# Kernel optimization log

Measured on AMD Instinct MI355X. Metric: run time of the kernel, lower is better.

The kernel has to match this reference:

```python
import jax, jax.numpy as jnp
import numpy as np

N_NODES = 100000


def _gcn_norm(edges, n_nodes):
    # PyG GCNConv: add self-loops, symmetric normalization D^{-1/2}(A+I)D^{-1/2}
    loop = jnp.arange(n_nodes, dtype=edges.dtype)
    src = jnp.concatenate([edges[0], loop])
    dst = jnp.concatenate([edges[1], loop])
    ones = jnp.ones(src.shape[0], dtype=jnp.float32)
    deg = jax.ops.segment_sum(ones, dst, num_segments=n_nodes)  # >=1 thanks to self-loops
    dinv = jax.lax.rsqrt(deg)
    norm = dinv[src] * dinv[dst]  # [E + N]
    return src, dst, norm


def _gcn_conv(x, W, b, src, dst, norm, n_nodes):
    # lin -> gather -> scale -> scatter-add -> +bias (PyG GCNConv order)
    h = x @ W                                   # [N, D_out]
    msg = h[src] * norm[:, None]                # [E+N, D_out]
    agg = jax.ops.segment_sum(msg, dst, num_segments=n_nodes)
    return agg + b


def setup_inputs() -> dict:
    key = jax.random.key(0)
    k_x, k_e, k_w1, k_w2 = jax.random.split(key, 4)
    F_in, D_hid, n_labels, n_edges = 128, 128, 32, 625000
    features = jax.random.normal(k_x, (N_NODES, F_in), dtype=jnp.float32)
    edges = jax.random.randint(k_e, (2, n_edges), 0, N_NODES, dtype=jnp.int64)
    W1 = jax.random.normal(k_w1, (F_in, D_hid), dtype=jnp.float32) / np.sqrt(F_in)
    b1 = jnp.zeros((D_hid,), dtype=jnp.float32)
    W2 = jax.random.normal(k_w2, (D_hid, n_labels), dtype=jnp.float32) / np.sqrt(D_hid)
    b2 = jnp.zeros((n_labels,), dtype=jnp.float32)
    return {"features": features, "edges": edges, "W1": W1, "b1": b1, "W2": W2, "b2": b2}


def reference(features, edges, W1, b1, W2, b2):
    n_nodes = features.shape[0]
    src, dst, norm = _gcn_norm(edges, n_nodes)
    h1 = jax.nn.relu(_gcn_conv(features, W1, b1, src, dst, norm, n_nodes))
    h2 = _gcn_conv(h1, W2, b2, src, dst, norm, n_nodes)
    return jax.nn.log_softmax(h2, axis=1)
```

## Files before the change

### kernel.cpp

```cpp
#include <hip/hip_runtime.h>

#define NN 100000
#define MAXDEG 64

typedef _Float16 f16;
typedef f16 f16x2 __attribute__((ext_vector_type(2)));
typedef f16 f16x8 __attribute__((ext_vector_type(8)));
typedef float f32x4 __attribute__((ext_vector_type(4)));

__device__ __forceinline__ int detect_is64(const void* edges, int E) {
    const long long* p = (const long long*)edges;
    int m = E < 1024 ? E : 1024;
    int bad = 0;
    for (int i = (threadIdx.x & 63); i < m; i += 64) {
        if ((unsigned long long)p[i] >= (unsigned long long)NN) bad = 1;
    }
    return !__any(bad);
}

__device__ __forceinline__ int edge_at(const void* e, long i, int is64) {
    return is64 ? (int)((const long long*)e)[i] : ((const int*)e)[i];
}

__global__ __launch_bounds__(256) void k_prep(const float* __restrict__ W1,
                                              const float* __restrict__ W2,
                                              f16* __restrict__ BT1,
                                              f16* __restrict__ BT2,
                                              int* __restrict__ deg, int n) {
    int t = blockIdx.x * blockDim.x + threadIdx.x;
    int stride = gridDim.x * blockDim.x;
    for (int i = t; i < n; i += stride) deg[i] = 0;
    for (int i = t; i < 128 * 128; i += stride) {
        int nn = i >> 7, kk = i & 127;
        BT1[i] = (f16)W1[kk * 128 + nn];
    }
    for (int i = t; i < 32 * 128; i += stride) {
        int nn = i >> 7, kk = i & 127;
        BT2[i] = (f16)W2[kk * 32 + nn];
    }
}

__global__ __launch_bounds__(256) void k_geb(const float* __restrict__ X,
                                             const f16* __restrict__ BT,
                                             f16* __restrict__ H, int n,
                                             const void* edges, int E,
                                             int* __restrict__ deg,
                                             int* __restrict__ csr,
                                             int nG, int nF) {
    __shared__ __align__(16) unsigned char Bs[16384];
    const int bid = blockIdx.x;
    const int lo = nG < nF ? nG : nF;
    int gid = -1, fid = -1;
    if (bid < 2 * lo) {
        if ((bid & 1) == 0) gid = bid >> 1; else fid = bid >> 1;
    } else if (nG > nF) {
        gid = bid - lo;
    } else {
        fid = bid - lo;
    }

    if (fid >= 0) {
        int is64 = detect_is64(edges, E);
        long stride = (long)nF * 256;
        for (long e = (long)fid * 256 + threadIdx.x; e < E; e += stride) {
            int s = edge_at(edges, e, is64);
            int d = edge_at(edges, (long)E + e, is64);
            int t = atomicAdd(&deg[d], 1);
            if (t < MAXDEG) csr[(long)d * MAXDEG + t] = s;
        }
        return;
    }

    const int tid = threadIdx.x;
    const int wave = tid >> 6;
    const int lane = tid & 63;
    const int lrow = lane & 15;
    const int kgrp = lane >> 4;
    const int row0 = gid * 64 + wave * 16;
    int arow = row0 + lrow;
    if (arow >= n) arow = n - 1;

    f16x8 a[4];
#pragma unroll
    for (int ks = 0; ks < 4; ks++) {
        const float* ap = &X[(long)arow * 128 + ks * 32 + kgrp * 8];
        float4 v0 = *(const float4*)ap;
        float4 v1 = *(const float4*)(ap + 4);
        f16x8 tv;
        tv[0] = (f16)v0.x; tv[1] = (f16)v0.y; tv[2] = (f16)v0.z; tv[3] = (f16)v0.w;
        tv[4] = (f16)v1.x; tv[5] = (f16)v1.y; tv[6] = (f16)v1.z; tv[7] = (f16)v1.w;
        a[ks] = tv;
    }

    const int sw = (lrow & 7) << 4;
#pragma unroll
    for (int half = 0; half < 2; half++) {
#pragma unroll
        for (int s = 0; s < 4; s++) {
            int L = (tid + s * 256) * 16;
            int row = L >> 8;
            f16x8 v = *(const f16x8*)((const unsigned char*)BT + half * 16384 + L);
            *(f16x8*)(Bs + (L ^ ((row & 7) << 4))) = v;
        }
        __syncthreads();
#pragma unroll
        for (int ntl = 0; ntl < 4; ntl++) {
            f32x4 acc = {0.f, 0.f, 0.f, 0.f};
            const int bbase = (ntl * 16 + lrow) * 256 + kgrp * 16;
#pragma unroll
            for (int ks = 0; ks < 4; ks++) {
                f16x8 b = *(const f16x8*)(Bs + ((bbase + ks * 64) ^ sw));
                acc = __builtin_amdgcn_mfma_f32_16x16x32_f16(a[ks], b, acc, 0, 0, 0);
            }
            const int col = (half * 4 + ntl) * 16 + lrow;
#pragma unroll
            for (int r = 0; r < 4; r++) {
                int grow = row0 + kgrp * 4 + r;
                if (grow < n) H[(long)grow * 128 + col] = (f16)acc[r];
            }
        }
        __syncthreads();
    }
}

__global__ __launch_bounds__(256) void k_gemm2(const f16* __restrict__ A,
                                               const f16* __restrict__ BT,
                                               f16* __restrict__ H, int n) {
    __shared__ __align__(16) unsigned char Bs[8192];
    const int tid = threadIdx.x;
    {
        int L = tid * 16;
        int row = L >> 8;
        f16x8 v = *(const f16x8*)((const unsigned char*)BT + L);
        *(f16x8*)(Bs + (L ^ ((row & 7) << 4))) = v;
        L += 4096; row = L >> 8;
        v = *(const f16x8*)((const unsigned char*)BT + L);
        *(f16x8*)(Bs + (L ^ ((row & 7) << 4))) = v;
    }
    __syncthreads();

    const int wave = tid >> 6;
    const int lane = tid & 63;
    const int lrow = lane & 15;
    const int kgrp = lane >> 4;
    const int row0 = blockIdx.x * 64 + wave * 16;
    if (row0 >= n) return;
    int arow = row0 + lrow;
    if (arow >= n) arow = n - 1;

    f16x8 a[4];
#pragma unroll
    for (int ks = 0; ks < 4; ks++)
        a[ks] = *(const f16x8*)&A[(long)arow * 128 + ks * 32 + kgrp * 8];

    const int sw = (lrow & 7) << 4;
#pragma unroll
    for (int nt = 0; nt < 2; nt++) {
        f32x4 acc = {0.f, 0.f, 0.f, 0.f};
        const int bbase = (nt * 16 + lrow) * 256 + kgrp * 16;
#pragma unroll
        for (int ks = 0; ks < 4; ks++) {
            f16x8 b = *(const f16x8*)(Bs + ((bbase + ks * 64) ^ sw));
            acc = __builtin_amdgcn_mfma_f32_16x16x32_f16(a[ks], b, acc, 0, 0, 0);
        }
        const int col = nt * 16 + lrow;
#pragma unroll
        for (int r = 0; r < 4; r++) {
            int grow = row0 + kgrp * 4 + r;
            if (grow < n) H[(long)grow * 32 + col] = (f16)acc[r];
        }
    }
}

__global__ __launch_bounds__(256) void k_spmm1(const f16* __restrict__ H,
                                               const int* __restrict__ deg,
                                               const int* __restrict__ csr,
                                               const float* __restrict__ b1,
                                               f16* __restrict__ O, int n) {
    const int lane = threadIdx.x & 15;
    const int nhw = (gridDim.x * blockDim.x) >> 4;
    const f16x8* H8 = (const f16x8*)H;
    const float4 bl = *(const float4*)&b1[lane * 8];
    const float4 bh = *(const float4*)&b1[lane * 8 + 4];
    for (int node = (blockIdx.x * blockDim.x + threadIdx.x) >> 4; node < n;
         node += nhw) {
        int dg = deg[node];
        float di = rsqrtf((float)(dg + 1));
        float w0 = di * di;
        f16x8 self = H8[(long)node * 16 + lane];
        float acc0[8], acc1[8], acc2[8], acc3[8];
#pragma unroll
        for (int j = 0; j < 8; j++) {
            acc0[j] = w0 * (float)self[j];
            acc1[j] = 0.f; acc2[j] = 0.f; acc3[j] = 0.f;
        }
        int s0 = node * MAXDEG;
        int s1 = s0 + (dg < MAXDEG ? dg : MAXDEG);
        int i = s0;
        for (; i + 4 <= s1; i += 4) {
            int sA = csr[i], sB = csr[i + 1], sC = csr[i + 2], sD = csr[i + 3];
            f16x8 vA = H8[(long)sA * 16 + lane];
            f16x8 vB = H8[(long)sB * 16 + lane];
            f16x8 vC = H8[(long)sC * 16 + lane];
            f16x8 vD = H8[(long)sD * 16 + lane];
            float wA = rsqrtf((float)(deg[sA] + 1)) * di;
            float wB = rsqrtf((float)(deg[sB] + 1)) * di;
            float wC = rsqrtf((float)(deg[sC] + 1)) * di;
            float wD = rsqrtf((float)(deg[sD] + 1)) * di;
#pragma unroll
            for (int j = 0; j < 8; j++) {
                acc0[j] += wA * (float)vA[j];
                acc1[j] += wB * (float)vB[j];
                acc2[j] += wC * (float)vC[j];
                acc3[j] += wD * (float)vD[j];
            }
        }
        for (; i < s1; i++) {
            int s = csr[i];
            float w = rsqrtf((float)(deg[s] + 1)) * di;
            f16x8 v = H8[(long)s * 16 + lane];
#pragma unroll
            for (int j = 0; j < 8; j++) acc0[j] += w * (float)v[j];
        }
        f16x8 o;
        o[0] = (f16)fmaxf(acc0[0] + acc1[0] + acc2[0] + acc3[0] + bl.x, 0.f);
        o[1] = (f16)fmaxf(acc0[1] + acc1[1] + acc2[1] + acc3[1] + bl.y, 0.f);
        o[2] = (f16)fmaxf(acc0[2] + acc1[2] + acc2[2] + acc3[2] + bl.z, 0.f);
        o[3] = (f16)fmaxf(acc0[3] + acc1[3] + acc2[3] + acc3[3] + bl.w, 0.f);
        o[4] = (f16)fmaxf(acc0[4] + acc1[4] + acc2[4] + acc3[4] + bh.x, 0.f);
        o[5] = (f16)fmaxf(acc0[5] + acc1[5] + acc2[5] + acc3[5] + bh.y, 0.f);
        o[6] = (f16)fmaxf(acc0[6] + acc1[6] + acc2[6] + acc3[6] + bh.z, 0.f);
        o[7] = (f16)fmaxf(acc0[7] + acc1[7] + acc2[7] + acc3[7] + bh.w, 0.f);
        ((f16x8*)O)[(long)node * 16 + lane] = o;
    }
}

__global__ __launch_bounds__(256) void k_spmm2(const f16* __restrict__ H,
                                               const int* __restrict__ deg,
                                               const int* __restrict__ csr,
                                               const float* __restrict__ b2,
                                               float* __restrict__ out, int n) {
    const int lane = threadIdx.x & 15;
    const int stot = (gridDim.x * blockDim.x) >> 4;
    const f16x2* H2 = (const f16x2*)H;
    const float2 bias = *(const float2*)&b2[lane * 2];
    for (int node = (blockIdx.x * blockDim.x + threadIdx.x) >> 4; node < n;
         node += stot) {
        int dg = deg[node];
        float di = rsqrtf((float)(dg + 1));
        float w0 = di * di;
        f16x2 self = H2[(long)node * 16 + lane];
        float a0 = w0 * (float)self[0], a1 = w0 * (float)self[1];
        float b0 = 0.f, b1v = 0.f, c0 = 0.f, c1 = 0.f, d0 = 0.f, d1 = 0.f;
        int s0 = node * MAXDEG;
        int s1 = s0 + (dg < MAXDEG ? dg : MAXDEG);
        int i = s0;
        for (; i + 4 <= s1; i += 4) {
            int sA = csr[i], sB = csr[i + 1], sC = csr[i + 2], sD = csr[i + 3];
            f16x2 vA = H2[(long)sA * 16 + lane];
            f16x2 vB = H2[(long)sB * 16 + lane];
            f16x2 vC = H2[(long)sC * 16 + lane];
            f16x2 vD = H2[(long)sD * 16 + lane];
            float wA = rsqrtf((float)(deg[sA] + 1)) * di;
            float wB = rsqrtf((float)(deg[sB] + 1)) * di;
            float wC = rsqrtf((float)(deg[sC] + 1)) * di;
            float wD = rsqrtf((float)(deg[sD] + 1)) * di;
            a0 += wA * (float)vA[0]; a1 += wA * (float)vA[1];
            b0 += wB * (float)vB[0]; b1v += wB * (float)vB[1];
            c0 += wC * (float)vC[0]; c1 += wC * (float)vC[1];
            d0 += wD * (float)vD[0]; d1 += wD * (float)vD[1];
        }
        for (; i < s1; i++) {
            int s = csr[i];
            float w = rsqrtf((float)(deg[s] + 1)) * di;
            f16x2 v = H2[(long)s * 16 + lane];
            a0 += w * (float)v[0]; a1 += w * (float)v[1];
        }
        float acc0 = a0 + b0 + c0 + d0 + bias.x;
        float acc1 = a1 + b1v + c1 + d1 + bias.y;
        float m = fmaxf(acc0, acc1);
#pragma unroll
        for (int off = 8; off >= 1; off >>= 1) m = fmaxf(m, __shfl_xor(m, off));
        float l = expf(acc0 - m) + expf(acc1 - m);
#pragma unroll
        for (int off = 8; off >= 1; off >>= 1) l += __shfl_xor(l, off);
        float lg = m + logf(l);
        *(float2*)&out[(long)node * 32 + lane * 2] =
            make_float2(acc0 - lg, acc1 - lg);
    }
}

extern "C" void kernel_launch(void* const* d_in, const int* in_sizes, int n_in,
                              void* d_out, int out_size, void* d_ws, size_t ws_size,
                              hipStream_t stream) {
    const float* X  = (const float*)d_in[0];
    const void* edges = d_in[1];
    const float* W1 = (const float*)d_in[2];
    const float* b1 = (const float*)d_in[3];
    const float* W2 = (const float*)d_in[4];
    const float* b2 = (const float*)d_in[5];
    float* out = (float*)d_out;

    const int n = in_sizes[0] / 128;
    const int E = in_sizes[1] / 2;

    char* w = (char*)d_ws;
    auto alloc = [&](size_t bytes) -> char* {
        char* p = w;
        w += (bytes + 511) & ~(size_t)511;
        return p;
    };
    int* deg = (int*)alloc((size_t)n * 4);
    int* csr = (int*)alloc((size_t)n * MAXDEG * 4);
    f16* BT1 = (f16*)alloc(128 * 128 * 2);
    f16* BT2 = (f16*)alloc(32 * 128 * 2);
    f16* h1  = (f16*)alloc((size_t)n * 128 * 2);
    f16* h1b = (f16*)alloc((size_t)n * 128 * 2);
    f16* h2  = (f16*)alloc((size_t)n * 32 * 2);

    k_prep<<<256, 256, 0, stream>>>(W1, W2, BT1, BT2, deg, n);

    const int nG = (n + 63) / 64;
    const int nF = 2048;
    k_geb<<<nG + nF, 256, 0, stream>>>(X, BT1, h1, n, edges, E, deg, csr, nG, nF);

    k_spmm1<<<2048, 256, 0, stream>>>(h1, deg, csr, b1, h1b, n);
    k_gemm2<<<(n + 63) / 64, 256, 0, stream>>>(h1b, BT2, h2, n);
    k_spmm2<<<2048, 256, 0, stream>>>(h2, deg, csr, b2, out, n);
}
```

Measured before the change: 112.7 us.

## Batch edge atomics four-way, use nontemporal stores, hoist degree loads, retune grids

The CSR-fill path now processes four edges per thread per iteration, issuing all loads and atomics before the stores, and writes CSR entries with nontemporal stores. The fill block count drops from 2048 to 512 so each thread does more work. In both SpMM kernels the neighbor degree loads are hoisted ahead of the feature gathers, and the final log-softmax output uses a nontemporal store. The prep grid is doubled. The aim is more memory-level parallelism and less cache pollution, at the cost of fewer fill blocks interleaved with the GEMM blocks.

```diff
diff --git a/kernel.cpp b/kernel.cpp
--- a/kernel.cpp
+++ b/kernel.cpp
@@ -7,6 +7,7 @@
 typedef f16 f16x2 __attribute__((ext_vector_type(2)));
 typedef f16 f16x8 __attribute__((ext_vector_type(8)));
 typedef float f32x4 __attribute__((ext_vector_type(4)));
+typedef float f32x2 __attribute__((ext_vector_type(2)));
 
 __device__ __forceinline__ int detect_is64(const void* edges, int E) {
     const long long* p = (const long long*)edges;
@@ -61,12 +62,23 @@
 
     if (fid >= 0) {
         int is64 = detect_is64(edges, E);
-        long stride = (long)nF * 256;
-        for (long e = (long)fid * 256 + threadIdx.x; e < E; e += stride) {
-            int s = edge_at(edges, e, is64);
-            int d = edge_at(edges, (long)E + e, is64);
-            int t = atomicAdd(&deg[d], 1);
-            if (t < MAXDEG) csr[(long)d * MAXDEG + t] = s;
+        const long T = (long)nF * 256;
+        for (long e = (long)fid * 256 + threadIdx.x; e < E; e += 4 * T) {
+            long e1 = e + T, e2 = e + 2 * T, e3 = e + 3 * T;
+            int s0 = edge_at(edges, e, is64);
+            int d0 = edge_at(edges, (long)E + e, is64);
+            int s1 = 0, d1 = -1, s2 = 0, d2 = -1, s3 = 0, d3 = -1;
+            if (e1 < E) { s1 = edge_at(edges, e1, is64); d1 = edge_at(edges, (long)E + e1, is64); }
+            if (e2 < E) { s2 = edge_at(edges, e2, is64); d2 = edge_at(edges, (long)E + e2, is64); }
+            if (e3 < E) { s3 = edge_at(edges, e3, is64); d3 = edge_at(edges, (long)E + e3, is64); }
+            int t0 = atomicAdd(&deg[d0], 1);
+            int t1 = (d1 >= 0) ? atomicAdd(&deg[d1], 1) : MAXDEG;
+            int t2 = (d2 >= 0) ? atomicAdd(&deg[d2], 1) : MAXDEG;
+            int t3 = (d3 >= 0) ? atomicAdd(&deg[d3], 1) : MAXDEG;
+            if (t0 < MAXDEG) __builtin_nontemporal_store(s0, &csr[(long)d0 * MAXDEG + t0]);
+            if (t1 < MAXDEG) __builtin_nontemporal_store(s1, &csr[(long)d1 * MAXDEG + t1]);
+            if (t2 < MAXDEG) __builtin_nontemporal_store(s2, &csr[(long)d2 * MAXDEG + t2]);
+            if (t3 < MAXDEG) __builtin_nontemporal_store(s3, &csr[(long)d3 * MAXDEG + t3]);
         }
         return;
     }
@@ -199,14 +211,15 @@
         int i = s0;
         for (; i + 4 <= s1; i += 4) {
             int sA = csr[i], sB = csr[i + 1], sC = csr[i + 2], sD = csr[i + 3];
+            int dA = deg[sA], dB = deg[sB], dC = deg[sC], dD = deg[sD];
             f16x8 vA = H8[(long)sA * 16 + lane];
             f16x8 vB = H8[(long)sB * 16 + lane];
             f16x8 vC = H8[(long)sC * 16 + lane];
             f16x8 vD = H8[(long)sD * 16 + lane];
-            float wA = rsqrtf((float)(deg[sA] + 1)) * di;
-            float wB = rsqrtf((float)(deg[sB] + 1)) * di;
-            float wC = rsqrtf((float)(deg[sC] + 1)) * di;
-            float wD = rsqrtf((float)(deg[sD] + 1)) * di;
+            float wA = rsqrtf((float)(dA + 1)) * di;
+            float wB = rsqrtf((float)(dB + 1)) * di;
+            float wC = rsqrtf((float)(dC + 1)) * di;
+            float wD = rsqrtf((float)(dD + 1)) * di;
 #pragma unroll
             for (int j = 0; j < 8; j++) {
                 acc0[j] += wA * (float)vA[j];
@@ -257,14 +270,15 @@
         int i = s0;
         for (; i + 4 <= s1; i += 4) {
             int sA = csr[i], sB = csr[i + 1], sC = csr[i + 2], sD = csr[i + 3];
+            int dA = deg[sA], dB = deg[sB], dC = deg[sC], dD = deg[sD];
             f16x2 vA = H2[(long)sA * 16 + lane];
             f16x2 vB = H2[(long)sB * 16 + lane];
             f16x2 vC = H2[(long)sC * 16 + lane];
             f16x2 vD = H2[(long)sD * 16 + lane];
-            float wA = rsqrtf((float)(deg[sA] + 1)) * di;
-            float wB = rsqrtf((float)(deg[sB] + 1)) * di;
-            float wC = rsqrtf((float)(deg[sC] + 1)) * di;
-            float wD = rsqrtf((float)(deg[sD] + 1)) * di;
+            float wA = rsqrtf((float)(dA + 1)) * di;
+            float wB = rsqrtf((float)(dB + 1)) * di;
+            float wC = rsqrtf((float)(dC + 1)) * di;
+            float wD = rsqrtf((float)(dD + 1)) * di;
             a0 += wA * (float)vA[0]; a1 += wA * (float)vA[1];
             b0 += wB * (float)vB[0]; b1v += wB * (float)vB[1];
             c0 += wC * (float)vC[0]; c1 += wC * (float)vC[1];
@@ -285,8 +299,8 @@
 #pragma unroll
         for (int off = 8; off >= 1; off >>= 1) l += __shfl_xor(l, off);
         float lg = m + logf(l);
-        *(float2*)&out[(long)node * 32 + lane * 2] =
-            make_float2(acc0 - lg, acc1 - lg);
+        f32x2 ov = {acc0 - lg, acc1 - lg};
+        __builtin_nontemporal_store(ov, (f32x2*)&out[(long)node * 32 + lane * 2]);
     }
 }
 
@@ -318,10 +332,10 @@
     f16* h1b = (f16*)alloc((size_t)n * 128 * 2);
     f16* h2  = (f16*)alloc((size_t)n * 32 * 2);
 
-    k_prep<<<256, 256, 0, stream>>>(W1, W2, BT1, BT2, deg, n);
+    k_prep<<<512, 256, 0, stream>>>(W1, W2, BT1, BT2, deg, n);
 
     const int nG = (n + 63) / 64;
-    const int nF = 2048;
+    const int nF = 512;
     k_geb<<<nG + nF, 256, 0, stream>>>(X, BT1, h1, n, edges, E, deg, csr, nG, nF);
 
     k_spmm1<<<2048, 256, 0, stream>>>(h1, deg, csr, b1, h1b, n);
```

Measured after the change: 122.3 us. 1.09x slower.
